# Optimization experiments

Hardware: AMD Instinct MI355X
Metric: run time of the kernel (lower is better)

Reference implementation:

```python
import jax, jax.numpy as jnp
import numpy as np

K = 1024
D = 256
DECAY = 0.99
EPS = 1e-05


def setup_inputs() -> dict:
    key = jax.random.key(0)
    k1, k2 = jax.random.split(key)
    z = jax.random.normal(k1, (16, 4096, D), dtype=jnp.float32)
    codebook = jax.random.normal(k2, (K, D), dtype=jnp.float32)
    cluster_size = jnp.zeros((K,), dtype=jnp.float32)
    embed_avg = jnp.zeros((K, D), dtype=jnp.float32)
    return {"z": z, "codebook": codebook, "cluster_size": cluster_size, "embed_avg": embed_avg}


def reference(z, codebook, cluster_size, embed_avg):
    B, S, d = z.shape
    z_flat = z.reshape(B * S, d)  # (BS, d)
    # L2 distances via ||z||^2 + ||c||^2 - 2 z.c  -> (BS, K)
    z_sq = jnp.sum(z_flat * z_flat, axis=1, keepdims=True)
    c_sq = jnp.sum(codebook * codebook, axis=1)[None, :]
    dist = z_sq + c_sq - 2.0 * (z_flat @ codebook.T)
    indices = jnp.argmin(dist, axis=1)  # (BS,)
    z_q = codebook[indices].reshape(B, S, d)
    # Straight-through estimator
    z_q_st = z + jax.lax.stop_gradient(z_q - z)
    # EMA codebook update (no-grad in original)
    counts = jax.ops.segment_sum(jnp.ones_like(indices, dtype=z.dtype), indices, num_segments=K)
    sums = jax.ops.segment_sum(z_flat, indices, num_segments=K)  # (K, d)
    new_cluster_size = cluster_size * DECAY + counts * (1.0 - DECAY)
    new_embed_avg = embed_avg * DECAY + sums * (1.0 - DECAY)
    new_codebook = new_embed_avg / (new_cluster_size + EPS)[:, None]
    return (z_q_st, indices.reshape(B, S), new_codebook, new_cluster_size, new_embed_avg)
```

## Files before the change

kernel.cpp:

```cpp
#include <hip/hip_runtime.h>

#define N_ROWS 65536
#define DIM    256
#define KCODES 1024

typedef _Float16 h8 __attribute__((ext_vector_type(8)));
typedef _Float16 h4 __attribute__((ext_vector_type(4)));
typedef float    f4 __attribute__((ext_vector_type(4)));

__global__ __launch_bounds__(64) void prep_csq(const float* __restrict__ cb,
                                               float* __restrict__ csq) {
    const int k = blockIdx.x;
    const int l = threadIdx.x;
    float4 v = reinterpret_cast<const float4*>(cb)[k * 64 + l];
    float s = v.x * v.x + v.y * v.y + v.z * v.z + v.w * v.w;
#pragma unroll
    for (int m = 32; m >= 1; m >>= 1) s += __shfl_xor(s, m, 64);
    if (l == 0) csq[k] = s;
}

__global__ __launch_bounds__(64) void prep_pack(const float* __restrict__ cb,
                                                _Float16* __restrict__ packB) {
    const int blk = blockIdx.x;
    const int G = blk >> 3, dc = blk & 7;
    const int l = threadIdx.x, lm = l & 15, lk = l >> 4;
#pragma unroll
    for (int j = 0; j < 8; ++j) {
        const int n = j >> 1, h = j & 1;
        const int code = G * 64 + n * 16 + lm;
        h8 v;
#pragma unroll
        for (int e = 0; e < 8; ++e) {
            const int d = dc * 32 + lk * 8 + e;
            float val = cb[code * 256 + d];
            _Float16 hi = (_Float16)val;
            v[e] = h ? (_Float16)(val - (float)hi) : hi;
        }
        *reinterpret_cast<h8*>(&packB[((blk * 8 + j) << 9) + (l << 3)]) = v;
    }
}

__global__ __launch_bounds__(512, 2) void vq_gemm(
    const float* __restrict__ z, const _Float16* __restrict__ packB,
    const float* __restrict__ csq_g,
    float* __restrict__ out_idx, int* __restrict__ idx_ws) {
    __shared__ _Float16 Ahi[128 * 256];
    __shared__ _Float16 Alo[128 * 256];
    __shared__ float csq_s[KCODES];
    __shared__ float red_val[128 * 4];
    __shared__ int   red_idx[128 * 4];

    const int t = threadIdx.x;
    const int row0 = blockIdx.x << 7;
    const int wave = t >> 6;
    const int wr  = wave >> 2;
    const int wcq = wave & 3;
    const int lane = t & 63;
    const int lm = lane & 15;
    const int lk = lane >> 4;

    csq_s[t]       = csq_g[t];
    csq_s[t + 512] = csq_g[t + 512];

    {
        const float4* z4 = reinterpret_cast<const float4*>(z) + (size_t)row0 * 64;
#pragma unroll
        for (int i = 0; i < 16; ++i) {
            int f = t + i * 512;
            int row = f >> 6, k4 = f & 63;
            float4 v = z4[f];
            h4 hv, lv;
            hv[0] = (_Float16)v.x; lv[0] = (_Float16)(v.x - (float)hv[0]);
            hv[1] = (_Float16)v.y; lv[1] = (_Float16)(v.y - (float)hv[1]);
            hv[2] = (_Float16)v.z; lv[2] = (_Float16)(v.z - (float)hv[2]);
            hv[3] = (_Float16)v.w; lv[3] = (_Float16)(v.w - (float)hv[3]);
            int idx = (row * 256 + k4 * 4) ^ ((row & 7) << 3);
            *reinterpret_cast<h4*>(&Ahi[idx]) = hv;
            *reinterpret_cast<h4*>(&Alo[idx]) = lv;
        }
    }
    __syncthreads();

    float bval[4][4];
    int   bidx[4][4];
#pragma unroll
    for (int m = 0; m < 4; ++m)
#pragma unroll
        for (int j = 0; j < 4; ++j) { bval[m][j] = 3.4e38f; bidx[m][j] = 0x7fffffff; }

    const f4 zacc = {0.0f, 0.0f, 0.0f, 0.0f};

    for (int o = 0; o < 4; ++o) {
        const int G = o * 4 + wcq;
        const _Float16* bbase = packB + ((size_t)G << 15);

        f4 acc[4][4];
#pragma unroll
        for (int m = 0; m < 4; ++m)
#pragma unroll
            for (int n = 0; n < 4; ++n) acc[m][n] = zacc;

        h8 bcur[8], bnxt[8];
#pragma unroll
        for (int j = 0; j < 8; ++j)
            bcur[j] = *reinterpret_cast<const h8*>(&bbase[(j << 9) + (lane << 3)]);

        for (int dc = 0; dc < 8; ++dc) {
            if (dc < 7) {
                const _Float16* bb = bbase + ((dc + 1) << 12);
#pragma unroll
                for (int j = 0; j < 8; ++j)
                    bnxt[j] = *reinterpret_cast<const h8*>(&bb[(j << 9) + (lane << 3)]);
            }
            h8 ah[4], al[4];
#pragma unroll
            for (int m = 0; m < 4; ++m) {
                int row = wr * 64 + m * 16 + lm;
                int idx = (row * 256 + dc * 32 + lk * 8) ^ ((row & 7) << 3);
                ah[m] = *reinterpret_cast<const h8*>(&Ahi[idx]);
                al[m] = *reinterpret_cast<const h8*>(&Alo[idx]);
            }
#pragma unroll
            for (int m = 0; m < 4; ++m)
#pragma unroll
                for (int n = 0; n < 4; ++n) {
                    acc[m][n] = __builtin_amdgcn_mfma_f32_16x16x32_f16(ah[m], bcur[n * 2 + 0], acc[m][n], 0, 0, 0);
                    acc[m][n] = __builtin_amdgcn_mfma_f32_16x16x32_f16(al[m], bcur[n * 2 + 0], acc[m][n], 0, 0, 0);
                    acc[m][n] = __builtin_amdgcn_mfma_f32_16x16x32_f16(ah[m], bcur[n * 2 + 1], acc[m][n], 0, 0, 0);
                }
#pragma unroll
            for (int j = 0; j < 8; ++j) bcur[j] = bnxt[j];
        }

#pragma unroll
        for (int n = 0; n < 4; ++n) {
            int code = o * 256 + wcq * 64 + n * 16 + lm;
            float cs = csq_s[code];
#pragma unroll
            for (int m = 0; m < 4; ++m)
#pragma unroll
                for (int j = 0; j < 4; ++j) {
                    float d = cs - 2.0f * acc[m][n][j];
                    if (d < bval[m][j] || (d == bval[m][j] && code < bidx[m][j])) {
                        bval[m][j] = d;
                        bidx[m][j] = code;
                    }
                }
        }
    }

#pragma unroll
    for (int s = 1; s <= 8; s <<= 1) {
#pragma unroll
        for (int m = 0; m < 4; ++m)
#pragma unroll
            for (int j = 0; j < 4; ++j) {
                float ov = __shfl_xor(bval[m][j], s, 64);
                int   oi = __shfl_xor(bidx[m][j], s, 64);
                if (ov < bval[m][j] || (ov == bval[m][j] && oi < bidx[m][j])) {
                    bval[m][j] = ov;
                    bidx[m][j] = oi;
                }
            }
    }
    if (lm == 0) {
#pragma unroll
        for (int m = 0; m < 4; ++m)
#pragma unroll
            for (int j = 0; j < 4; ++j) {
                int rl = wr * 64 + m * 16 + lk * 4 + j;
                red_val[rl * 4 + wcq] = bval[m][j];
                red_idx[rl * 4 + wcq] = bidx[m][j];
            }
    }
    __syncthreads();
    if (t < 128) {
        float bv = red_val[t * 4];
        int   bi = red_idx[t * 4];
#pragma unroll
        for (int w = 1; w < 4; ++w) {
            float v = red_val[t * 4 + w];
            int   i2 = red_idx[t * 4 + w];
            if (v < bv || (v == bv && i2 < bi)) { bv = v; bi = i2; }
        }
        out_idx[row0 + t] = (float)bi;
        idx_ws[row0 + t] = bi;
    }
}

__global__ __launch_bounds__(256) void hist_kernel(const int* __restrict__ idx_ws,
                                                   int* __restrict__ counts_i) {
    __shared__ int h[KCODES];
    const int t = threadIdx.x;
#pragma unroll
    for (int i = 0; i < 4; ++i) h[t + i * 256] = 0;
    __syncthreads();
    atomicAdd(&h[idx_ws[blockIdx.x * 256 + t]], 1);
    __syncthreads();
#pragma unroll
    for (int i = 0; i < 4; ++i) {
        int c = h[t + i * 256];
        if (c) atomicAdd(&counts_i[t + i * 256], c);
    }
}

__global__ __launch_bounds__(1024) void scan_kernel(const int* __restrict__ counts_i,
                                                    int* __restrict__ offsets,
                                                    int* __restrict__ cursor) {
    __shared__ int a[KCODES], b[KCODES];
    const int t = threadIdx.x;
    int cnt = counts_i[t];
    a[t] = cnt;
    __syncthreads();
    int* src = a; int* dst = b;
    for (int s = 1; s < 1024; s <<= 1) {
        dst[t] = (t >= s) ? (src[t - s] + src[t]) : src[t];
        __syncthreads();
        int* tmp = src; src = dst; dst = tmp;
    }
    int excl = src[t] - cnt;
    offsets[t] = excl;
    cursor[t] = excl;
}

__global__ __launch_bounds__(256) void place_kernel(const int* __restrict__ idx_ws,
                                                    int* __restrict__ cursor,
                                                    int* __restrict__ perm) {
    const int r = blockIdx.x * 256 + threadIdx.x;
    const int c = idx_ws[r];
    const int pos = atomicAdd(&cursor[c], 1);
    perm[pos] = r;
}

__global__ __launch_bounds__(256) void segsum_partial(
    const float* __restrict__ z, const int* __restrict__ perm,
    const int* __restrict__ idx_ws, float* __restrict__ sums) {
    __shared__ int srow[32];
    __shared__ int scode[32];
    const int t = threadIdx.x;
    const int base = blockIdx.x << 5;
    if (t < 32) {
        int r = perm[base + t];
        srow[t] = r;
        scode[t] = idx_ws[r];
    }
    __syncthreads();
    float s = z[(size_t)srow[0] * 256 + t];
    int cur = scode[0];
#pragma unroll 8
    for (int i = 1; i < 32; ++i) {
        int c = scode[i];
        float v = z[(size_t)srow[i] * 256 + t];
        if (c != cur) {
            atomicAdd(&sums[cur * 256 + t], s);
            s = v; cur = c;
        } else {
            s += v;
        }
    }
    atomicAdd(&sums[cur * 256 + t], s);
}

__global__ __launch_bounds__(256) void ema_kernel(
    const float* __restrict__ cluster_size, const float* __restrict__ embed_avg,
    const float* __restrict__ sums, const int* __restrict__ counts_i,
    float* __restrict__ out_cb, float* __restrict__ out_cs, float* __restrict__ out_ea) {
    const int k = blockIdx.x, d = threadIdx.x;
    const float ncs = cluster_size[k] * 0.99f + (float)counts_i[k] * 0.01f;
    const int o = k * 256 + d;
    const float nea = embed_avg[o] * 0.99f + sums[o] * 0.01f;
    out_ea[o] = nea;
    out_cb[o] = nea / (ncs + 1e-5f);
    if (d == 0) out_cs[k] = ncs;
}

__global__ __launch_bounds__(256) void ste_kernel(const float* __restrict__ z,
                                                  const float* __restrict__ cb,
                                                  const int* __restrict__ idx_ws,
                                                  float* __restrict__ out_zq) {
    __shared__ int sidx[32];
    const int t = threadIdx.x;
    const int r0 = blockIdx.x << 5;
    if (t < 32) sidx[t] = idx_ws[r0 + t];
    __syncthreads();
    const int rs = t >> 6;
    const int c4 = t & 63;
#pragma unroll 1
    for (int it = 0; it < 8; ++it) {
        int r = it * 4 + rs;
        int bk = sidx[r];
        float4 zv = reinterpret_cast<const float4*>(z)[(size_t)(r0 + r) * 64 + c4];
        float4 cv = reinterpret_cast<const float4*>(cb)[bk * 64 + c4];
        float4 ov;
        ov.x = zv.x + (cv.x - zv.x);
        ov.y = zv.y + (cv.y - zv.y);
        ov.z = zv.z + (cv.z - zv.z);
        ov.w = zv.w + (cv.w - zv.w);
        reinterpret_cast<float4*>(out_zq)[(size_t)(r0 + r) * 64 + c4] = ov;
    }
}

extern "C" void kernel_launch(void* const* d_in, const int* in_sizes, int n_in,
                              void* d_out, int out_size, void* d_ws, size_t ws_size,
                              hipStream_t stream) {
    const float* z            = (const float*)d_in[0];
    const float* cb           = (const float*)d_in[1];
    const float* cluster_size = (const float*)d_in[2];
    const float* embed_avg    = (const float*)d_in[3];

    float* out_zq  = (float*)d_out;
    float* out_idx = out_zq + (size_t)N_ROWS * DIM;
    float* out_cb  = out_idx + N_ROWS;
    float* out_cs  = out_cb + (size_t)KCODES * DIM;
    float* out_ea  = out_cs + KCODES;

    char* w = (char*)d_ws;
    _Float16* packB = (_Float16*)w;   w += (size_t)KCODES * DIM * 2 * 2;
    float* csq      = (float*)w;      w += (size_t)KCODES * 4;
    int* idx_ws     = (int*)w;        w += (size_t)N_ROWS * 4;
    int* counts_i   = (int*)w;        w += (size_t)KCODES * 4;
    int* offsets    = (int*)w;        w += (size_t)KCODES * 4;
    int* cursor     = (int*)w;        w += (size_t)KCODES * 4;
    int* perm       = (int*)w;        w += (size_t)N_ROWS * 4;
    float* sums     = (float*)w;

    hipMemsetAsync(counts_i, 0, KCODES * sizeof(int), stream);
    hipMemsetAsync(sums, 0, (size_t)KCODES * DIM * sizeof(float), stream);
    prep_csq<<<KCODES, 64, 0, stream>>>(cb, csq);
    prep_pack<<<128, 64, 0, stream>>>(cb, packB);
    vq_gemm<<<N_ROWS / 128, 512, 0, stream>>>(z, packB, csq, out_idx, idx_ws);
    hist_kernel<<<N_ROWS / 256, 256, 0, stream>>>(idx_ws, counts_i);
    scan_kernel<<<1, 1024, 0, stream>>>(counts_i, offsets, cursor);
    place_kernel<<<N_ROWS / 256, 256, 0, stream>>>(idx_ws, cursor, perm);
    segsum_partial<<<N_ROWS / 32, 256, 0, stream>>>(z, perm, idx_ws, sums);
    ema_kernel<<<KCODES, 256, 0, stream>>>(cluster_size, embed_avg, sums, counts_i,
                                           out_cb, out_cs, out_ea);
    ste_kernel<<<N_ROWS / 32, 256, 0, stream>>>(z, cb, idx_ws, out_zq);
}
```

Baseline: 432.1 us.

## Remap vq_gemm waves to 4x2 grid with smaller per-wave tiles, drop B prefetch

Changes the wave layout in the distance GEMM from a 2x4 (rows x code groups) split to a 4x2 split. Each wave now covers 32 rows and iterates over 8 code groups of 64 instead of 4, which halves the accumulator and argmin register state. The software double-buffered B prefetch is removed in favour of direct per-chunk global loads. The aim is lower VGPR pressure, so the kernel can hold occupancy and issue MFMAs more freely, at the cost of more B traffic per wave and less latency hiding on global loads.

```diff
diff --git a/kernel.cpp b/kernel.cpp
--- a/kernel.cpp
+++ b/kernel.cpp
@@ -39,6 +39,8 @@
         *reinterpret_cast<h8*>(&packB[((blk * 8 + j) << 9) + (l << 3)]) = v;
     }
 }
+
+#define MF(A, B, C) C = __builtin_amdgcn_mfma_f32_16x16x32_f16(A, B, C, 0, 0, 0)
 
 __global__ __launch_bounds__(512, 2) void vq_gemm(
     const float* __restrict__ z, const _Float16* __restrict__ packB,
@@ -47,14 +49,14 @@
     __shared__ _Float16 Ahi[128 * 256];
     __shared__ _Float16 Alo[128 * 256];
     __shared__ float csq_s[KCODES];
-    __shared__ float red_val[128 * 4];
-    __shared__ int   red_idx[128 * 4];
+    __shared__ float red_val[128 * 2];
+    __shared__ int   red_idx[128 * 2];
 
     const int t = threadIdx.x;
     const int row0 = blockIdx.x << 7;
     const int wave = t >> 6;
-    const int wr  = wave >> 2;
-    const int wcq = wave & 3;
+    const int wr = wave >> 1;
+    const int wc = wave & 1;
     const int lane = t & 63;
     const int lm = lane & 15;
     const int lk = lane >> 4;
@@ -81,63 +83,65 @@
     }
     __syncthreads();
 
-    float bval[4][4];
-    int   bidx[4][4];
-#pragma unroll
-    for (int m = 0; m < 4; ++m)
+    float bval[2][4];
+    int   bidx[2][4];
+#pragma unroll
+    for (int m = 0; m < 2; ++m)
 #pragma unroll
         for (int j = 0; j < 4; ++j) { bval[m][j] = 3.4e38f; bidx[m][j] = 0x7fffffff; }
 
     const f4 zacc = {0.0f, 0.0f, 0.0f, 0.0f};
 
-    for (int o = 0; o < 4; ++o) {
-        const int G = o * 4 + wcq;
-        const _Float16* bbase = packB + ((size_t)G << 15);
-
-        f4 acc[4][4];
-#pragma unroll
-        for (int m = 0; m < 4; ++m)
+    const int r0_ = wr * 32 + lm;
+    const int r1_ = r0_ + 16;
+    const int sw  = (r0_ & 7) << 3;
+    const int aoff0 = r0_ * 256 + lk * 8;
+    const int aoff1 = r1_ * 256 + lk * 8;
+
+    for (int o = 0; o < 8; ++o) {
+        const int G = o * 2 + wc;
+        const h8* bb8 = reinterpret_cast<const h8*>(packB) + ((size_t)G << 12) + lane;
+
+        f4 acc[2][4];
+#pragma unroll
+        for (int m = 0; m < 2; ++m)
 #pragma unroll
             for (int n = 0; n < 4; ++n) acc[m][n] = zacc;
 
-        h8 bcur[8], bnxt[8];
-#pragma unroll
-        for (int j = 0; j < 8; ++j)
-            bcur[j] = *reinterpret_cast<const h8*>(&bbase[(j << 9) + (lane << 3)]);
-
         for (int dc = 0; dc < 8; ++dc) {
-            if (dc < 7) {
-                const _Float16* bb = bbase + ((dc + 1) << 12);
-#pragma unroll
-                for (int j = 0; j < 8; ++j)
-                    bnxt[j] = *reinterpret_cast<const h8*>(&bb[(j << 9) + (lane << 3)]);
-            }
-            h8 ah[4], al[4];
-#pragma unroll
-            for (int m = 0; m < 4; ++m) {
-                int row = wr * 64 + m * 16 + lm;
-                int idx = (row * 256 + dc * 32 + lk * 8) ^ ((row & 7) << 3);
-                ah[m] = *reinterpret_cast<const h8*>(&Ahi[idx]);
-                al[m] = *reinterpret_cast<const h8*>(&Alo[idx]);
-            }
-#pragma unroll
-            for (int m = 0; m < 4; ++m)
-#pragma unroll
-                for (int n = 0; n < 4; ++n) {
-                    acc[m][n] = __builtin_amdgcn_mfma_f32_16x16x32_f16(ah[m], bcur[n * 2 + 0], acc[m][n], 0, 0, 0);
-                    acc[m][n] = __builtin_amdgcn_mfma_f32_16x16x32_f16(al[m], bcur[n * 2 + 0], acc[m][n], 0, 0, 0);
-                    acc[m][n] = __builtin_amdgcn_mfma_f32_16x16x32_f16(ah[m], bcur[n * 2 + 1], acc[m][n], 0, 0, 0);
-                }
-#pragma unroll
-            for (int j = 0; j < 8; ++j) bcur[j] = bnxt[j];
+            const h8* bp = bb8 + (dc << 9);
+            h8 b0 = bp[0];
+            h8 b1 = bp[64];
+            h8 b2 = bp[128];
+            h8 b3 = bp[192];
+            h8 b4 = bp[256];
+            h8 b5 = bp[320];
+            h8 b6 = bp[384];
+            h8 b7 = bp[448];
+
+            const int i0 = (aoff0 + dc * 32) ^ sw;
+            const int i1 = (aoff1 + dc * 32) ^ sw;
+            h8 ah0 = *reinterpret_cast<const h8*>(&Ahi[i0]);
+            h8 al0 = *reinterpret_cast<const h8*>(&Alo[i0]);
+            h8 ah1 = *reinterpret_cast<const h8*>(&Ahi[i1]);
+            h8 al1 = *reinterpret_cast<const h8*>(&Alo[i1]);
+
+            MF(ah0, b0, acc[0][0]); MF(al0, b0, acc[0][0]); MF(ah0, b1, acc[0][0]);
+            MF(ah1, b0, acc[1][0]); MF(al1, b0, acc[1][0]); MF(ah1, b1, acc[1][0]);
+            MF(ah0, b2, acc[0][1]); MF(al0, b2, acc[0][1]); MF(ah0, b3, acc[0][1]);
+            MF(ah1, b2, acc[1][1]); MF(al1, b2, acc[1][1]); MF(ah1, b3, acc[1][1]);
+            MF(ah0, b4, acc[0][2]); MF(al0, b4, acc[0][2]); MF(ah0, b5, acc[0][2]);
+            MF(ah1, b4, acc[1][2]); MF(al1, b4, acc[1][2]); MF(ah1, b5, acc[1][2]);
+            MF(ah0, b6, acc[0][3]); MF(al0, b6, acc[0][3]); MF(ah0, b7, acc[0][3]);
+            MF(ah1, b6, acc[1][3]); MF(al1, b6, acc[1][3]); MF(ah1, b7, acc[1][3]);
         }
 
 #pragma unroll
         for (int n = 0; n < 4; ++n) {
-            int code = o * 256 + wcq * 64 + n * 16 + lm;
+            int code = G * 64 + n * 16 + lm;
             float cs = csq_s[code];
 #pragma unroll
-            for (int m = 0; m < 4; ++m)
+            for (int m = 0; m < 2; ++m)
 #pragma unroll
                 for (int j = 0; j < 4; ++j) {
                     float d = cs - 2.0f * acc[m][n][j];
@@ -152,7 +156,7 @@
 #pragma unroll
     for (int s = 1; s <= 8; s <<= 1) {
 #pragma unroll
-        for (int m = 0; m < 4; ++m)
+        for (int m = 0; m < 2; ++m)
 #pragma unroll
             for (int j = 0; j < 4; ++j) {
                 float ov = __shfl_xor(bval[m][j], s, 64);
@@ -165,24 +169,21 @@
     }
     if (lm == 0) {
 #pragma unroll
-        for (int m = 0; m < 4; ++m)
+        for (int m = 0; m < 2; ++m)
 #pragma unroll
             for (int j = 0; j < 4; ++j) {
-                int rl = wr * 64 + m * 16 + lk * 4 + j;
-                red_val[rl * 4 + wcq] = bval[m][j];
-                red_idx[rl * 4 + wcq] = bidx[m][j];
+                int rl = wr * 32 + m * 16 + lk * 4 + j;
+                red_val[rl * 2 + wc] = bval[m][j];
+                red_idx[rl * 2 + wc] = bidx[m][j];
             }
     }
     __syncthreads();
     if (t < 128) {
-        float bv = red_val[t * 4];
-        int   bi = red_idx[t * 4];
-#pragma unroll
-        for (int w = 1; w < 4; ++w) {
-            float v = red_val[t * 4 + w];
-            int   i2 = red_idx[t * 4 + w];
-            if (v < bv || (v == bv && i2 < bi)) { bv = v; bi = i2; }
-        }
+        float bv = red_val[t * 2];
+        int   bi = red_idx[t * 2];
+        float v = red_val[t * 2 + 1];
+        int   i2 = red_idx[t * 2 + 1];
+        if (v < bv || (v == bv && i2 < bi)) { bv = v; bi = i2; }
         out_idx[row0 + t] = (float)bi;
         idx_ws[row0 + t] = bi;
     }
```

Result: faster. 349.4 us (-19.1%).
